# Kernel optimization log

Measured on AMD Instinct MI355X. Metric: run time of the kernel, lower is better.

Reference implementation:

```python
import jax, jax.numpy as jnp
import numpy as np

B, T, C, H = 2, 2048, 1024, 16
HD = C // H  # head dim = 64


def setup_inputs() -> dict:
    key = jax.random.key(0)
    k0, k1, k2 = jax.random.split(key, 3)
    x = jax.random.normal(k0, (B, T, C), jnp.float32)
    W_attn = jax.random.normal(k1, (C, 3 * C), jnp.float32) * 0.02
    b_attn = jnp.zeros((3 * C,), jnp.float32)
    W_proj = jax.random.normal(k2, (C, C), jnp.float32) * 0.02
    b_proj = jnp.zeros((C,), jnp.float32)
    # causal mask, broadcast over (B, H) like torch masked_fill(~mask)
    attn_mask = jnp.tril(jnp.ones((T, T), dtype=bool))[None, None]
    return {"x": x, "W_attn": W_attn, "b_attn": b_attn,
            "W_proj": W_proj, "b_proj": b_proj, "attn_mask": attn_mask}


def _rotate_half(x):
    # interleaved rotate_half as in rotary-embedding-torch: (x1,x2)->(-x2,x1)
    x1 = x[..., 0::2]
    x2 = x[..., 1::2]
    return jnp.stack((-x2, x1), axis=-1).reshape(x.shape)


def _apply_rope(x):
    # x: [B, H, T, HD]
    hd = x.shape[-1]
    t = x.shape[-2]
    inv_freq = 1.0 / (10000.0 ** (jnp.arange(0, hd, 2, dtype=jnp.float32) / hd))
    freqs = jnp.arange(t, dtype=jnp.float32)[:, None] * inv_freq[None, :]  # [T, HD/2]
    freqs = jnp.repeat(freqs, 2, axis=-1)  # [T, HD], interleaved
    return x * jnp.cos(freqs) + _rotate_half(x) * jnp.sin(freqs)


def reference(x, W_attn, b_attn, W_proj, b_proj, attn_mask):
    Bb, Tt, Cc = x.shape
    qkv = x @ W_attn + b_attn                     # [B, T, 3C]
    q, k, v = jnp.split(qkv, 3, axis=-1)

    def to_heads(z):
        return z.reshape(Bb, Tt, H, HD).transpose(0, 2, 1, 3)  # [B, H, T, HD]

    q, k, v = to_heads(q), to_heads(k), to_heads(v)
    q = _apply_rope(q)
    k = _apply_rope(k)

    scale = 1.0 / jnp.sqrt(jnp.float32(HD))
    att = jnp.einsum('bhqd,bhkd->bhqk', q, k) * scale  # [B, H, T, T]
    att = jnp.where(attn_mask, att, jnp.float32(-10000.0))
    att = jax.nn.softmax(att, axis=-1)
    # dropout = 0.0 (eval): identity
    y = jnp.einsum('bhqk,bhkd->bhqd', att, v)           # [B, H, T, HD]
    y = y.transpose(0, 2, 1, 3).reshape(Bb, Tt, Cc)
    return y @ W_proj + b_proj
```

## Files before the change

kernel.cpp:

```cpp
#include <hip/hip_runtime.h>

#define B_ 2
#define T_ 2048
#define C_ 1024
#define H_ 16
#define HD_ 64

typedef unsigned short u16;
typedef unsigned int u32;
typedef __attribute__((ext_vector_type(8))) short short8;
typedef __attribute__((ext_vector_type(4))) float f32x4;
typedef __attribute__((ext_vector_type(2))) u32 uint2v;
typedef __attribute__((ext_vector_type(4))) u32 uint4v;

typedef __attribute__((address_space(1))) const void* as1cv;
typedef __attribute__((address_space(3))) void* as3v;

__device__ __forceinline__ u16 f2bf(float x){
  union { float f; u32 u; } v; v.f = x;
  u32 r = v.u + 0x7fffu + ((v.u >> 16) & 1u);
  return (u16)(r >> 16);
}
__device__ __forceinline__ float bf2f(u16 h){
  union { u32 u; float f; } v; v.u = ((u32)h) << 16;
  return v.f;
}
__device__ __forceinline__ u32 cvt_pk_bf16(float lo, float hi){
  u32 r;
  asm("v_cvt_pk_bf16_f32 %0, %1, %2" : "=v"(r) : "v"(lo), "v"(hi));
  return r;
}
__device__ __forceinline__ void gl_lds16(const u16* src, u16* dst){
  __builtin_amdgcn_global_load_lds((as1cv)src, (as3v)dst, 16, 0, 0);
}

__global__ void k_conv(const float* __restrict__ in, u16* __restrict__ out){
  int i = blockIdx.x * 256 + threadIdx.x;
  f32x4 v = ((const f32x4*)in)[i];
  uint2v o;
  o.x = (u32)f2bf(v.x) | ((u32)f2bf(v.y) << 16);
  o.y = (u32)f2bf(v.z) | ((u32)f2bf(v.w) << 16);
  ((uint2v*)out)[i] = o;
}

__global__ void k_transpose(const float* __restrict__ in, u16* __restrict__ out,
                            int R, int Cc){
  __shared__ float tile[32][33];
  int c0 = blockIdx.x * 32, r0 = blockIdx.y * 32;
  int tx = threadIdx.x, ty = threadIdx.y;
#pragma unroll
  for (int ii = 0; ii < 4; ++ii)
    tile[ty + ii*8][tx] = in[(size_t)(r0 + ty + ii*8) * Cc + c0 + tx];
  __syncthreads();
#pragma unroll
  for (int ii = 0; ii < 4; ++ii)
    out[(size_t)(c0 + ty + ii*8) * R + r0 + tx] = f2bf(tile[tx][ty + ii*8]);
}

__global__ __launch_bounds__(256, 3)
void k_gemm0(const u16* __restrict__ A, const u16* __restrict__ Bt,
             const float* __restrict__ bias, u16* __restrict__ Qh,
             u16* __restrict__ Kh, u16* __restrict__ vt,
             int M, int N, int K)
{
  __shared__ u16 As[128*64];
  __shared__ u16 Bs[128*64];
  int nwg = gridDim.x;
  int cpx = nwg >> 3;
  int bid = blockIdx.x;
  int wg = (bid & 7) * cpx + (bid >> 3);
  int ntn = N >> 7;
  int m0 = (wg / ntn) << 7, n0 = (wg % ntn) << 7;
  int tid = threadIdx.x;
  int lane = tid & 63, w = tid >> 6;
  int c = lane & 15, g = lane >> 4;
  int wr = w >> 1, wc = w & 1;

  f32x4 z4 = {0.f,0.f,0.f,0.f};
  f32x4 acc[4][4];
#pragma unroll
  for (int i=0;i<4;++i)
#pragma unroll
    for (int j=0;j<4;++j) acc[i][j] = z4;

  u16* dstA = As + ((tid & 0xC0) << 3);
  u16* dstB = Bs + ((tid & 0xC0) << 3);

  for (int k0 = 0; k0 < K; k0 += 64){
#pragma unroll
    for (int it = 0; it < 4; ++it){
      int ch = it*256 + tid;
      int row = ch >> 3, slot = ch & 7;
      gl_lds16(A + (size_t)(m0+row)*K + k0 + slot*8, dstA + it*2048);
    }
#pragma unroll
    for (int it = 0; it < 4; ++it){
      int ch = it*256 + tid;
      int row = ch >> 3, slot = ch & 7;
      gl_lds16(Bt + (size_t)(n0+row)*K + k0 + slot*8, dstB + it*2048);
    }
    __syncthreads();
#pragma unroll
    for (int ks = 0; ks < 2; ++ks){
      short8 af[4], bf[4];
#pragma unroll
      for (int i=0;i<4;++i)
        af[i] = *(const short8*)(As + (wr*64 + i*16 + c)*64 + ks*32 + g*8);
#pragma unroll
      for (int j=0;j<4;++j)
        bf[j] = *(const short8*)(Bs + (wc*64 + j*16 + c)*64 + ks*32 + g*8);
#pragma unroll
      for (int i=0;i<4;++i)
#pragma unroll
        for (int j=0;j<4;++j)
          acc[i][j] = __builtin_amdgcn_mfma_f32_16x16x32_bf16(af[i], bf[j], acc[i][j], 0, 0, 0);
    }
    __syncthreads();
  }

  if (n0 >= 2048){
#pragma unroll
    for (int i=0;i<4;++i){
      int rowb = m0 + wr*64 + i*16 + g*4;
      int bb = rowb >> 11, t0 = rowb & 2047;
#pragma unroll
      for (int j=0;j<4;++j){
        int col = n0 + wc*64 + j*16 + c;
        float bv = bias[col];
        int vc = col - 2048;
        int hh = vc >> 6, d = vc & 63;
        uint2v o;
        o.x = (u32)f2bf(acc[i][j].x + bv) | ((u32)f2bf(acc[i][j].y + bv) << 16);
        o.y = (u32)f2bf(acc[i][j].z + bv) | ((u32)f2bf(acc[i][j].w + bv) << 16);
        *(uint2v*)(vt + ((size_t)((bb*16 + hh)*64 + d))*2048 + t0) = o;
      }
    }
  } else {
    bool isQ = (n0 < 1024);
    u16* dsth = isQ ? Qh : Kh;
    int colb = isQ ? n0 : (n0 - 1024);
    float qsc = isQ ? 0.180336880f : 1.0f;
    float sgn = (c & 1) ? 1.f : -1.f;
#pragma unroll
    for (int nf=0; nf<4; ++nf){
      int scol = colb + wc*64 + nf*16 + c;
      int hh = scol >> 6, d = scol & 63;
      int ip = (d >> 1);
      float invr = exp2f((float)(-ip) * 0.4152410118609203f) * 0.15915494309f;
      float bv = bias[n0 + wc*64 + nf*16 + c];
      u16* base = dsth + (size_t)hh*2048*64 + d;
#pragma unroll
      for (int mf=0; mf<4; ++mf){
#pragma unroll
        for (int r=0; r<4; ++r){
          int row = m0 + wr*64 + mf*16 + g*4 + r;
          int t = row & 2047, b = row >> 11;
          float v = acc[mf][nf][r] + bv;
          float p = __shfl_xor(v, 1);
          float th = (float)t * invr;
          float fr = th - floorf(th);
          float sn = __builtin_amdgcn_sinf(fr);
          float cs = __builtin_amdgcn_cosf(fr);
          float y = (v*cs + p*sn*sgn) * qsc;
          base[((size_t)b*16*2048 + t)*64] = f2bf(y);
        }
      }
    }
  }
}

__global__ __launch_bounds__(256, 2)
void k_gemmp(const u16* __restrict__ A, const u16* __restrict__ Bt,
             const float* __restrict__ bias, float* __restrict__ outf)
{
  __shared__ u16 LDSG[32768];
  const int K = 1024, N = 1024;
  int nwg = gridDim.x;
  int cpx = nwg >> 3;
  int bid = blockIdx.x;
  int wg = (bid & 7) * cpx + (bid >> 3);
  int m0 = (wg >> 3) << 7, n0 = (wg & 7) << 7;
  int tid = threadIdx.x;
  int lane = tid & 63, w = tid >> 6;
  int c = lane & 15, g = lane >> 4;
  int wr = w >> 1, wc = w & 1;

  f32x4 z4 = {0.f,0.f,0.f,0.f};
  f32x4 acc[4][4];
#pragma unroll
  for (int i=0;i<4;++i)
#pragma unroll
    for (int j=0;j<4;++j) acc[i][j] = z4;

  int rowS[4], slotS[4], dstS[4];
#pragma unroll
  for (int it=0; it<4; ++it){
    int ch = it*256 + tid;
    rowS[it] = ch >> 3;
    slotS[it] = (ch & 7) * 8;
    dstS[it] = it*2048 + ((tid & 0xC0) << 3);
  }
  const u16* Abase = A + (size_t)m0*K;
  const u16* Bbase = Bt + (size_t)n0*K;

#pragma unroll
  for (int it=0; it<4; ++it){
    gl_lds16(Abase + (size_t)rowS[it]*K + slotS[it], LDSG + dstS[it]);
    gl_lds16(Bbase + (size_t)rowS[it]*K + slotS[it], LDSG + 16384 + dstS[it]);
  }
  __syncthreads();

  const int nk = K >> 6;
  for (int kt = 0; kt < nk; ++kt){
    int cur = kt & 1;
    if (kt + 1 < nk){
      int k1 = (kt + 1) << 6;
      int nb = cur ^ 1;
#pragma unroll
      for (int it=0; it<4; ++it){
        gl_lds16(Abase + (size_t)rowS[it]*K + k1 + slotS[it], LDSG + nb*8192 + dstS[it]);
        gl_lds16(Bbase + (size_t)rowS[it]*K + k1 + slotS[it], LDSG + 16384 + nb*8192 + dstS[it]);
      }
    }
    const u16* As = LDSG + cur*8192;
    const u16* Bs = LDSG + 16384 + cur*8192;
#pragma unroll
    for (int ks = 0; ks < 2; ++ks){
      short8 af[4], bf[4];
#pragma unroll
      for (int i=0;i<4;++i)
        af[i] = *(const short8*)(As + (wr*64 + i*16 + c)*64 + ks*32 + g*8);
#pragma unroll
      for (int j=0;j<4;++j)
        bf[j] = *(const short8*)(Bs + (wc*64 + j*16 + c)*64 + ks*32 + g*8);
#pragma unroll
      for (int i=0;i<4;++i)
#pragma unroll
        for (int j=0;j<4;++j)
          acc[i][j] = __builtin_amdgcn_mfma_f32_16x16x32_bf16(af[i], bf[j], acc[i][j], 0, 0, 0);
    }
    __syncthreads();
  }

#pragma unroll
  for (int i=0;i<4;++i){
#pragma unroll
    for (int j=0;j<4;++j){
      int col = n0 + wc*64 + j*16 + c;
      float bv = bias[col];
#pragma unroll
      for (int r=0;r<4;++r){
        int row = m0 + wr*64 + i*16 + g*4 + r;
        outf[(size_t)row*N + col] = acc[i][j][r] + bv;
      }
    }
  }
}

__global__ __launch_bounds__(256, 3)
void k_attn(const u16* __restrict__ Qh, const u16* __restrict__ Kh,
            const u16* __restrict__ Vt, u16* __restrict__ Pb,
            float* __restrict__ lp)
{
  __shared__ u16 KV[4*4096];
  __shared__ u16 Ps[4*32*64];

  int bid = blockIdx.x;
  int qt = 15 - (bid >> 7);
  int r7 = bid & 127;
  int ck = r7 >> 5, bh = r7 & 31;
  int q0 = qt << 7;
  int tid = threadIdx.x, lane = tid & 63, w = tid >> 6;
  int c = lane & 15, g = lane >> 4;
  int q0w = q0 + w*32;
  int nt = (qt + 1) << 1;
  int t0 = (nt * ck) >> 2;
  int t1 = (nt * (ck + 1)) >> 2;

  const u16* Kbase = Kh + (size_t)bh * T_ * 64;
  const u16* Vbase = Vt + (size_t)bh * 64 * T_;
  const u16* Qbase = Qh + (size_t)bh * T_ * 64;

  short8 qf[2][2];
#pragma unroll
  for (int qs=0;qs<2;++qs)
#pragma unroll
    for (int ks=0;ks<2;++ks)
      qf[qs][ks] = *(const short8*)(Qbase + (size_t)(q0w + qs*16 + c)*64 + ks*32 + g*8);

  f32x4 z4 = {0.f,0.f,0.f,0.f};
  f32x4 acc[2][4];
#pragma unroll
  for (int qs=0;qs<2;++qs)
#pragma unroll
    for (int ds=0;ds<4;++ds) acc[qs][ds] = z4;
  float psum[2] = {0.f, 0.f};

  char* PsB = (char*)Ps + w*4096;

  int row2[2], soff2[2];
  u16* dst0[2];
#pragma unroll
  for (int it=0; it<2; ++it){
    int ch = it*256 + tid;
    row2[it] = ch >> 3;
    int slot = ch & 7;
    soff2[it] = (slot ^ (row2[it] & 7)) << 3;
    dst0[it] = KV + ((it*256 + (tid & 0xC0)) << 3);
  }

  if (t0 < t1){
    int kv0 = t0 << 6;
#pragma unroll
    for (int it=0; it<2; ++it){
      gl_lds16(Kbase + (size_t)(kv0 + row2[it])*64 + soff2[it], dst0[it]);
      gl_lds16(Vbase + (size_t)row2[it]*T_ + kv0 + soff2[it], dst0[it] + 2*4096);
    }
  }
  __syncthreads();

  for (int t = t0; t < t1; ++t){
    int cur = (t - t0) & 1;
    int kv0 = t << 6;
    if (t + 1 < t1){
      int kvn = kv0 + 64;
      int nxt = cur ^ 1;
#pragma unroll
      for (int it=0; it<2; ++it){
        gl_lds16(Kbase + (size_t)(kvn + row2[it])*64 + soff2[it], dst0[it] + nxt*4096);
        gl_lds16(Vbase + (size_t)row2[it]*T_ + kvn + soff2[it], dst0[it] + (2+nxt)*4096);
      }
    }

    if (kv0 <= q0w + 31){
      const char* KsC = (const char*)(KV + cur*4096);
      const char* VsC = (const char*)(KV + (2+cur)*4096);

      f32x4 st[4][2];
#pragma unroll
      for (int kv=0;kv<4;++kv)
#pragma unroll
        for (int qs=0;qs<2;++qs) st[kv][qs] = z4;

#pragma unroll
      for (int ks=0;ks<2;++ks){
        short8 kf[4];
#pragma unroll
        for (int kv=0;kv<4;++kv){
          int row = kv*16 + c;
          kf[kv] = *(const short8*)(KsC + row*128 + (((ks*4+g) ^ (row&7)) << 4));
        }
#pragma unroll
        for (int kv=0;kv<4;++kv)
#pragma unroll
          for (int qs=0;qs<2;++qs)
            st[kv][qs] = __builtin_amdgcn_mfma_f32_16x16x32_bf16(kf[kv], qf[qs][ks], st[kv][qs], 0, 0, 0);
      }

      if (kv0 + 63 > q0w){
#pragma unroll
        for (int kv=0;kv<4;++kv)
#pragma unroll
          for (int qs=0;qs<2;++qs)
#pragma unroll
            for (int r=0;r<4;++r){
              int kvi = kv0 + kv*16 + g*4 + r;
              int qi = q0w + qs*16 + c;
              if (kvi > qi) st[kv][qs][r] = -INFINITY;
            }
      }

#pragma unroll
      for (int qs=0;qs<2;++qs){
        float s01 = 0.f, s23 = 0.f;
#pragma unroll
        for (int kv=0;kv<4;++kv){
          float e0 = __builtin_amdgcn_exp2f(st[kv][qs][0]);
          float e1 = __builtin_amdgcn_exp2f(st[kv][qs][1]);
          float e2 = __builtin_amdgcn_exp2f(st[kv][qs][2]);
          float e3 = __builtin_amdgcn_exp2f(st[kv][qs][3]);
          st[kv][qs][0] = e0; st[kv][qs][1] = e1;
          st[kv][qs][2] = e2; st[kv][qs][3] = e3;
          s01 += e0 + e1; s23 += e2 + e3;
        }
        psum[qs] += s01 + s23;
        int q = qs*16 + c;
#pragma unroll
        for (int kv=0;kv<4;++kv){
          uint2v o;
          o.x = cvt_pk_bf16(st[kv][qs][0], st[kv][qs][1]);
          o.y = cvt_pk_bf16(st[kv][qs][2], st[kv][qs][3]);
          *(uint2v*)(PsB + q*128 + ((kv*32 + g*8) ^ ((q&7) << 4))) = o;
        }
      }

#pragma unroll
      for (int ks=0;ks<2;++ks){
        short8 vb[4];
#pragma unroll
        for (int ds=0;ds<4;++ds){
          int row = ds*16 + c;
          vb[ds] = *(const short8*)(VsC + row*128 + (((ks*4+g) ^ (row&7)) << 4));
        }
#pragma unroll
        for (int qs=0;qs<2;++qs){
          int q = qs*16 + c;
          short8 pa = *(const short8*)(PsB + q*128 + (((ks*4+g) << 4) ^ ((q&7) << 4)));
#pragma unroll
          for (int ds=0;ds<4;++ds)
            acc[qs][ds] = __builtin_amdgcn_mfma_f32_16x16x32_bf16(pa, vb[ds], acc[qs][ds], 0, 0, 0);
        }
      }
    }

    __syncthreads();
  }

#pragma unroll
  for (int qs=0;qs<2;++qs){
    psum[qs] += __shfl_xor(psum[qs], 16);
    psum[qs] += __shfl_xor(psum[qs], 32);
  }
  if (g == 0){
    lp[ck*65536 + bh*2048 + q0w + c]      = psum[0];
    lp[ck*65536 + bh*2048 + q0w + 16 + c] = psum[1];
  }
#pragma unroll
  for (int qs=0;qs<2;++qs){
#pragma unroll
    for (int r=0;r<4;++r){
      int trow = q0w + qs*16 + g*4 + r;
      size_t off = (((size_t)(ck*32 + bh)*2048) + trow)*64;
#pragma unroll
      for (int ds=0;ds<4;++ds)
        Pb[off + ds*16 + c] = f2bf(acc[qs][ds][r]);
    }
  }
}

__global__ void k_merge(const u16* __restrict__ Pb, const float* __restrict__ lp,
                        u16* __restrict__ Y)
{
  int idx = blockIdx.x * 256 + threadIdx.x;
  int d8 = idx & 7;
  int t  = (idx >> 3) & 2047;
  int bh = idx >> 14;
  int lt = bh*2048 + t;
  float l = lp[lt] + lp[lt + 65536] + lp[lt + 131072] + lp[lt + 196608];
  float inv = 1.0f / l;
  float s[8] = {0.f,0.f,0.f,0.f,0.f,0.f,0.f,0.f};
#pragma unroll
  for (int ck=0; ck<4; ++ck){
    short8 p = *(const short8*)(Pb + (((size_t)(ck*32 + bh)*2048 + t) << 6) + d8*8);
#pragma unroll
    for (int j=0;j<8;++j) s[j] += bf2f((u16)p[j]);
  }
  uint4v o;
  o.x = cvt_pk_bf16(s[0]*inv, s[1]*inv);
  o.y = cvt_pk_bf16(s[2]*inv, s[3]*inv);
  o.z = cvt_pk_bf16(s[4]*inv, s[5]*inv);
  o.w = cvt_pk_bf16(s[6]*inv, s[7]*inv);
  int bb = bh >> 4, hh = bh & 15;
  *(uint4v*)(Y + ((size_t)(bb*2048 + t))*1024 + hh*64 + d8*8) = o;
}

extern "C" void kernel_launch(void* const* d_in, const int* in_sizes, int n_in,
                              void* d_out, int out_size, void* d_ws, size_t ws_size,
                              hipStream_t stream)
{
  const float* x  = (const float*)d_in[0];
  const float* Wa = (const float*)d_in[1];
  const float* ba = (const float*)d_in[2];
  const float* Wp = (const float*)d_in[3];
  const float* bp = (const float*)d_in[4];
  float* out = (float*)d_out;
  char* ws = (char*)d_ws;

  u16* xb  = (u16*)(ws);
  u16* WaT = (u16*)(ws + (8u  << 20));
  u16* Pb  = (u16*)(ws);
  u16* Qh  = (u16*)(ws + (32u << 20));
  u16* Y   = Qh;
  u16* Kh  = (u16*)(ws + (40u << 20));
  u16* Vt  = (u16*)(ws + (48u << 20));
  u16* WpT = (u16*)(ws + (56u << 20));
  float* lp = (float*)(ws + (58u << 20));

  k_conv<<<4096, 256, 0, stream>>>(x, xb);
  k_transpose<<<dim3(96,32), dim3(32,8), 0, stream>>>(Wa, WaT, 1024, 3072);
  k_transpose<<<dim3(32,32), dim3(32,8), 0, stream>>>(Wp, WpT, 1024, 1024);
  k_gemm0<<<768, 256, 0, stream>>>(xb, WaT, ba, Qh, Kh, Vt, 4096, 3072, 1024);
  k_attn<<<2048, 256, 0, stream>>>(Qh, Kh, Vt, Pb, lp);
  k_merge<<<2048, 256, 0, stream>>>(Pb, lp, Y);
  k_gemmp<<<256, 256, 0, stream>>>(Y, WpT, bp, out);
}
```

Before: 108.4 us.

## Vary attention KV split count by query tile and halve projection GEMM tile

The attention kernel now splits the KV range into 4, 2 or 1 chunks depending on the query tile's causal length, instead of always 4. This removes empty or tiny split blocks for early query tiles, so the grid shrinks from 2048 to 1760 blocks. The merge kernel reads and sums only the partials that exist for each tile. The output projection GEMM uses 64-row tiles with 512 blocks and higher occupancy to fill more CUs, at the cost of re-reading the B operand more often.

New measurement: 107.3 us. About the same (-1.1%).

```diff
diff --git a/kernel.cpp b/kernel.cpp
--- a/kernel.cpp
+++ b/kernel.cpp
@@ -169,45 +169,54 @@
   }
 }
 
-__global__ __launch_bounds__(256, 2)
+__global__ __launch_bounds__(256, 3)
 void k_gemmp(const u16* __restrict__ A, const u16* __restrict__ Bt,
              const float* __restrict__ bias, float* __restrict__ outf)
 {
-  __shared__ u16 LDSG[32768];
+  __shared__ u16 LDSG[24576];
   const int K = 1024, N = 1024;
   int nwg = gridDim.x;
   int cpx = nwg >> 3;
   int bid = blockIdx.x;
   int wg = (bid & 7) * cpx + (bid >> 3);
-  int m0 = (wg >> 3) << 7, n0 = (wg & 7) << 7;
+  int m0 = (wg >> 3) << 6, n0 = (wg & 7) << 7;
   int tid = threadIdx.x;
   int lane = tid & 63, w = tid >> 6;
   int c = lane & 15, g = lane >> 4;
   int wr = w >> 1, wc = w & 1;
 
   f32x4 z4 = {0.f,0.f,0.f,0.f};
-  f32x4 acc[4][4];
-#pragma unroll
-  for (int i=0;i<4;++i)
+  f32x4 acc[2][4];
+#pragma unroll
+  for (int i=0;i<2;++i)
 #pragma unroll
     for (int j=0;j<4;++j) acc[i][j] = z4;
 
-  int rowS[4], slotS[4], dstS[4];
+  int rowA[2], slotA[2], dstA[2];
+#pragma unroll
+  for (int it=0; it<2; ++it){
+    int ch = it*256 + tid;
+    rowA[it] = ch >> 3;
+    slotA[it] = (ch & 7) * 8;
+    dstA[it] = it*2048 + ((tid & 0xC0) << 3);
+  }
+  int rowB[4], slotB[4], dstB[4];
 #pragma unroll
   for (int it=0; it<4; ++it){
     int ch = it*256 + tid;
-    rowS[it] = ch >> 3;
-    slotS[it] = (ch & 7) * 8;
-    dstS[it] = it*2048 + ((tid & 0xC0) << 3);
+    rowB[it] = ch >> 3;
+    slotB[it] = (ch & 7) * 8;
+    dstB[it] = 8192 + it*2048 + ((tid & 0xC0) << 3);
   }
   const u16* Abase = A + (size_t)m0*K;
   const u16* Bbase = Bt + (size_t)n0*K;
 
 #pragma unroll
-  for (int it=0; it<4; ++it){
-    gl_lds16(Abase + (size_t)rowS[it]*K + slotS[it], LDSG + dstS[it]);
-    gl_lds16(Bbase + (size_t)rowS[it]*K + slotS[it], LDSG + 16384 + dstS[it]);
-  }
+  for (int it=0; it<2; ++it)
+    gl_lds16(Abase + (size_t)rowA[it]*K + slotA[it], LDSG + dstA[it]);
+#pragma unroll
+  for (int it=0; it<4; ++it)
+    gl_lds16(Bbase + (size_t)rowB[it]*K + slotB[it], LDSG + dstB[it]);
   __syncthreads();
 
   const int nk = K >> 6;
@@ -217,24 +226,25 @@
       int k1 = (kt + 1) << 6;
       int nb = cur ^ 1;
 #pragma unroll
-      for (int it=0; it<4; ++it){
-        gl_lds16(Abase + (size_t)rowS[it]*K + k1 + slotS[it], LDSG + nb*8192 + dstS[it]);
-        gl_lds16(Bbase + (size_t)rowS[it]*K + k1 + slotS[it], LDSG + 16384 + nb*8192 + dstS[it]);
-      }
-    }
-    const u16* As = LDSG + cur*8192;
-    const u16* Bs = LDSG + 16384 + cur*8192;
+      for (int it=0; it<2; ++it)
+        gl_lds16(Abase + (size_t)rowA[it]*K + k1 + slotA[it], LDSG + nb*4096 + dstA[it]);
+#pragma unroll
+      for (int it=0; it<4; ++it)
+        gl_lds16(Bbase + (size_t)rowB[it]*K + k1 + slotB[it], LDSG + nb*8192 + dstB[it]);
+    }
+    const u16* As = LDSG + cur*4096;
+    const u16* Bs = LDSG + 8192 + cur*8192;
 #pragma unroll
     for (int ks = 0; ks < 2; ++ks){
-      short8 af[4], bf[4];
-#pragma unroll
-      for (int i=0;i<4;++i)
-        af[i] = *(const short8*)(As + (wr*64 + i*16 + c)*64 + ks*32 + g*8);
+      short8 af[2], bf[4];
+#pragma unroll
+      for (int i=0;i<2;++i)
+        af[i] = *(const short8*)(As + (wr*32 + i*16 + c)*64 + ks*32 + g*8);
 #pragma unroll
       for (int j=0;j<4;++j)
         bf[j] = *(const short8*)(Bs + (wc*64 + j*16 + c)*64 + ks*32 + g*8);
 #pragma unroll
-      for (int i=0;i<4;++i)
+      for (int i=0;i<2;++i)
 #pragma unroll
         for (int j=0;j<4;++j)
           acc[i][j] = __builtin_amdgcn_mfma_f32_16x16x32_bf16(af[i], bf[j], acc[i][j], 0, 0, 0);
@@ -243,14 +253,14 @@
   }
 
 #pragma unroll
-  for (int i=0;i<4;++i){
+  for (int i=0;i<2;++i){
 #pragma unroll
     for (int j=0;j<4;++j){
       int col = n0 + wc*64 + j*16 + c;
       float bv = bias[col];
 #pragma unroll
       for (int r=0;r<4;++r){
-        int row = m0 + wr*64 + i*16 + g*4 + r;
+        int row = m0 + wr*32 + i*16 + g*4 + r;
         outf[(size_t)row*N + col] = acc[i][j][r] + bv;
       }
     }
@@ -266,16 +276,22 @@
   __shared__ u16 Ps[4*32*64];
 
   int bid = blockIdx.x;
-  int qt = 15 - (bid >> 7);
-  int r7 = bid & 127;
-  int ck = r7 >> 5, bh = r7 & 31;
+  int qt, ck, bh, l2nsp;
+  if (bid < 1536){
+    qt = 15 - (bid >> 7); ck = (bid >> 5) & 3; bh = bid & 31; l2nsp = 2;
+  } else if (bid < 1728){
+    int x = bid - 1536;
+    qt = 3 - (x >> 6); ck = (x >> 5) & 1; bh = x & 31; l2nsp = 1;
+  } else {
+    qt = 0; ck = 0; bh = (bid - 1728) & 31; l2nsp = 0;
+  }
   int q0 = qt << 7;
   int tid = threadIdx.x, lane = tid & 63, w = tid >> 6;
   int c = lane & 15, g = lane >> 4;
   int q0w = q0 + w*32;
   int nt = (qt + 1) << 1;
-  int t0 = (nt * ck) >> 2;
-  int t1 = (nt * (ck + 1)) >> 2;
+  int t0 = (nt * ck) >> l2nsp;
+  int t1 = (nt * (ck + 1)) >> l2nsp;
 
   const u16* Kbase = Kh + (size_t)bh * T_ * 64;
   const u16* Vbase = Vt + (size_t)bh * 64 * T_;
@@ -309,7 +325,7 @@
     dst0[it] = KV + ((it*256 + (tid & 0xC0)) << 3);
   }
 
-  if (t0 < t1){
+  {
     int kv0 = t0 << 6;
 #pragma unroll
     for (int it=0; it<2; ++it){
@@ -445,16 +461,29 @@
   int d8 = idx & 7;
   int t  = (idx >> 3) & 2047;
   int bh = idx >> 14;
+  int qt = t >> 7;
   int lt = bh*2048 + t;
-  float l = lp[lt] + lp[lt + 65536] + lp[lt + 131072] + lp[lt + 196608];
+  float s[8];
+  float l = lp[lt];
+  {
+    short8 p = *(const short8*)(Pb + (((size_t)bh*2048 + t) << 6) + d8*8);
+#pragma unroll
+    for (int j=0;j<8;++j) s[j] = bf2f((u16)p[j]);
+  }
+  if (qt >= 1){
+    l += lp[lt + 65536];
+    short8 p = *(const short8*)(Pb + (((size_t)(32 + bh)*2048 + t) << 6) + d8*8);
+#pragma unroll
+    for (int j=0;j<8;++j) s[j] += bf2f((u16)p[j]);
+  }
+  if (qt >= 4){
+    l += lp[lt + 131072] + lp[lt + 196608];
+    short8 p2 = *(const short8*)(Pb + (((size_t)(64 + bh)*2048 + t) << 6) + d8*8);
+    short8 p3 = *(const short8*)(Pb + (((size_t)(96 + bh)*2048 + t) << 6) + d8*8);
+#pragma unroll
+    for (int j=0;j<8;++j) s[j] += bf2f((u16)p2[j]) + bf2f((u16)p3[j]);
+  }
   float inv = 1.0f / l;
-  float s[8] = {0.f,0.f,0.f,0.f,0.f,0.f,0.f,0.f};
-#pragma unroll
-  for (int ck=0; ck<4; ++ck){
-    short8 p = *(const short8*)(Pb + (((size_t)(ck*32 + bh)*2048 + t) << 6) + d8*8);
-#pragma unroll
-    for (int j=0;j<8;++j) s[j] += bf2f((u16)p[j]);
-  }
   uint4v o;
   o.x = cvt_pk_bf16(s[0]*inv, s[1]*inv);
   o.y = cvt_pk_bf16(s[2]*inv, s[3]*inv);
@@ -490,7 +519,7 @@
   k_transpose<<<dim3(96,32), dim3(32,8), 0, stream>>>(Wa, WaT, 1024, 3072);
   k_transpose<<<dim3(32,32), dim3(32,8), 0, stream>>>(Wp, WpT, 1024, 1024);
   k_gemm0<<<768, 256, 0, stream>>>(xb, WaT, ba, Qh, Kh, Vt, 4096, 3072, 1024);
-  k_attn<<<2048, 256, 0, stream>>>(Qh, Kh, Vt, Pb, lp);
+  k_attn<<<1760, 256, 0, stream>>>(Qh, Kh, Vt, Pb, lp);
   k_merge<<<2048, 256, 0, stream>>>(Pb, lp, Y);
-  k_gemmp<<<256, 256, 0, stream>>>(Y, WpT, bp, out);
-}
+  k_gemmp<<<512, 256, 0, stream>>>(Y, WpT, bp, out);
+}
```
